# Kernel tuning notes

Hardware: AMD Instinct MI355X
Metric: run time of the kernel (lower is better)

Reference implementation:

```python
import jax, jax.numpy as jnp
import numpy as np

WS = 16          # window_size
SHIFT = 8        # shift_size
HEADS = 6
DIM = 180
CONV_SCALE = 0.01
EPS = 1e-5       # LayerNorm eps (torch default)


def _ln(x, g, b):
    mu = jnp.mean(x, -1, keepdims=True)
    var = jnp.mean((x - mu) ** 2, -1, keepdims=True)
    return (x - mu) / jnp.sqrt(var + EPS) * g + b


def _window_partition(x, ws):
    b, h, w, c = x.shape
    x = x.reshape(b, h // ws, ws, w // ws, ws, c)
    return x.transpose(0, 1, 3, 2, 4, 5).reshape(-1, ws, ws, c)


def _window_reverse(win, ws, h, w):
    b = win.shape[0] // ((h // ws) * (w // ws))
    x = win.reshape(b, h // ws, w // ws, ws, ws, -1)
    return x.transpose(0, 1, 3, 2, 4, 5).reshape(b, h, w, -1)


def _conv2d(x, w, b, pad):
    y = jax.lax.conv_general_dilated(x, w, (1, 1), ((pad, pad), (pad, pad)),
                                     dimension_numbers=('NCHW', 'OIHW', 'NCHW'))
    return y + b[None, :, None, None]


def setup_inputs() -> dict:
    key = jax.random.key(0)
    ks = jax.random.split(key, 12)
    b, h, w = 1, 256, 256
    c = DIM
    hid = int(c * 4.0)
    cr = c // 3     # compress_ratio=3
    sq = c // 30    # squeeze_factor=30
    x = jax.random.normal(ks[0], (b, h * w, c), jnp.float32)

    # relative position index (standard Swin recipe)
    coords = np.stack(np.meshgrid(np.arange(WS), np.arange(WS), indexing='ij')).reshape(2, -1)
    rel = (coords[:, :, None] - coords[:, None, :]).transpose(1, 2, 0)
    rel[:, :, 0] += WS - 1
    rel[:, :, 1] += WS - 1
    rel[:, :, 0] *= 2 * WS - 1
    rpi_sa = jnp.asarray(rel.sum(-1), jnp.int32)  # [ws*ws, ws*ws]

    # shifted-window attention mask
    img = np.zeros((h, w))
    cnt = 0
    for hs in (slice(0, -WS), slice(-WS, -SHIFT), slice(-SHIFT, None)):
        for wsl in (slice(0, -WS), slice(-WS, -SHIFT), slice(-SHIFT, None)):
            img[hs, wsl] = cnt
            cnt += 1
    mw = img.reshape(h // WS, WS, w // WS, WS).transpose(0, 2, 1, 3).reshape(-1, WS * WS)
    am = mw[:, None, :] - mw[:, :, None]
    attn_mask = jnp.asarray(np.where(am != 0, -100.0, 0.0), jnp.float32)  # [nW, n, n]

    def p(k, shape, std=0.02):
        return jax.random.normal(k, shape, jnp.float32) * std

    return dict(
        x=x, h=h, w=w, rpi_sa=rpi_sa, attn_mask=attn_mask,
        norm1_g=jnp.ones((c,), jnp.float32), norm1_b=jnp.zeros((c,), jnp.float32),
        qkv_w=p(ks[1], (c, 3 * c)), qkv_b=jnp.zeros((3 * c,), jnp.float32),
        rpb_table=p(ks[2], ((2 * WS - 1) * (2 * WS - 1), HEADS)),
        proj_w=p(ks[3], (c, c)), proj_b=jnp.zeros((c,), jnp.float32),
        conv1_w=p(ks[4], (cr, c, 3, 3)), conv1_b=jnp.zeros((cr,), jnp.float32),
        conv2_w=p(ks[5], (c, cr, 3, 3)), conv2_b=jnp.zeros((c,), jnp.float32),
        ca1_w=p(ks[6], (sq, c, 1, 1)), ca1_b=jnp.zeros((sq,), jnp.float32),
        ca2_w=p(ks[7], (c, sq, 1, 1)), ca2_b=jnp.zeros((c,), jnp.float32),
        norm2_g=jnp.ones((c,), jnp.float32), norm2_b=jnp.zeros((c,), jnp.float32),
        fc1_w=p(ks[8], (c, hid)), fc1_b=jnp.zeros((hid,), jnp.float32),
        fc2_w=p(ks[9], (hid, c)), fc2_b=jnp.zeros((c,), jnp.float32),
    )


def reference(x, h, w, rpi_sa, attn_mask,
              norm1_g, norm1_b, qkv_w, qkv_b, rpb_table, proj_w, proj_b,
              conv1_w, conv1_b, conv2_w, conv2_b, ca1_w, ca1_b, ca2_w, ca2_b,
              norm2_g, norm2_b, fc1_w, fc1_b, fc2_w, fc2_b):
    b, _, c = x.shape
    shortcut = x
    xn = _ln(x, norm1_g, norm1_b).reshape(b, h, w, c)

    # CAB conv branch (NCHW)
    xi = xn.transpose(0, 3, 1, 2)
    y = _conv2d(xi, conv1_w, conv1_b, 1)
    y = jax.nn.gelu(y, approximate=False)
    y = _conv2d(y, conv2_w, conv2_b, 1)
    ca = jnp.mean(y, axis=(2, 3), keepdims=True)          # AdaptiveAvgPool2d(1)
    ca = jax.nn.relu(_conv2d(ca, ca1_w, ca1_b, 0))
    ca = jax.nn.sigmoid(_conv2d(ca, ca2_w, ca2_b, 0))
    conv_x = (y * ca).transpose(0, 2, 3, 1).reshape(b, h * w, c)

    # shifted window attention
    sx = jnp.roll(xn, (-SHIFT, -SHIFT), (1, 2))
    xw = _window_partition(sx, WS).reshape(-1, WS * WS, c)  # [B_, n, c]
    B_, n, _ = xw.shape
    hd = c // HEADS
    qkv = (xw @ qkv_w + qkv_b).reshape(B_, n, 3, HEADS, hd).transpose(2, 0, 3, 1, 4)
    q, k, v = qkv[0] * hd ** (-0.5), qkv[1], qkv[2]
    attn = jnp.einsum('bhqd,bhkd->bhqk', q, k)
    rpb = rpb_table[rpi_sa.reshape(-1)].reshape(n, n, HEADS).transpose(2, 0, 1)
    attn = attn + rpb[None]
    nw = attn_mask.shape[0]
    attn = attn.reshape(B_ // nw, nw, HEADS, n, n) + attn_mask[None, :, None]
    attn = jax.nn.softmax(attn.reshape(B_, HEADS, n, n), -1)
    out = jnp.einsum('bhqk,bhkd->bhqd', attn, v).transpose(0, 2, 1, 3).reshape(B_, n, c)
    out = out @ proj_w + proj_b
    sx = _window_reverse(out.reshape(-1, WS, WS, c), WS, h, w)
    attn_x = jnp.roll(sx, (SHIFT, SHIFT), (1, 2)).reshape(b, h * w, c)

    x = shortcut + attn_x + conv_x * CONV_SCALE
    xm = _ln(x, norm2_g, norm2_b)
    m = jax.nn.gelu(xm @ fc1_w + fc1_b, approximate=False)
    x = x + (m @ fc2_w + fc2_b)
    return x
```

## Files before the change

### kernel.cpp

```cpp
#include <hip/hip_runtime.h>
#include <hip/hip_bf16.h>
#include <math.h>

#define NTOK 65536
#define C 180
#define KP1 192
#define RCHUNK 32768

typedef __attribute__((ext_vector_type(8))) __bf16 bf16x8;
typedef __attribute__((ext_vector_type(4))) float floatx4;

__device__ __forceinline__ float gelu_f(float v) {
    return 0.5f * v * (1.f + erff(v * 0.7071067811865475f));
}
__device__ __forceinline__ float bflo(unsigned int u) { return __uint_as_float(u << 16); }
__device__ __forceinline__ float bfhi(unsigned int u) { return __uint_as_float(u & 0xffff0000u); }

__device__ __forceinline__ int win2pix(int wrow) {
    int wi = wrow >> 8, ni = wrow & 255;
    int r2 = ((wi >> 4) << 4) | (ni >> 4);
    int c2 = ((wi & 15) << 4) | (ni & 15);
    int r = (r2 + 8) & 255, c = (c2 + 8) & 255;
    return (r << 8) | c;
}

__global__ __launch_bounds__(256) void ln_k(const float* __restrict__ x,
                                            const float* __restrict__ g,
                                            const float* __restrict__ b,
                                            __hip_bfloat16* __restrict__ y) {
    const int wav = threadIdx.x >> 6;
    const int lane = threadIdx.x & 63;
    const int row = blockIdx.x * 4 + wav;
    const float* xr = x + (size_t)row * C;
    float v0 = xr[lane];
    float v1 = xr[lane + 64];
    float v2 = (lane < C - 128) ? xr[lane + 128] : 0.f;
    float sum = v0 + v1 + v2;
    float sq = v0 * v0 + v1 * v1 + v2 * v2;
#pragma unroll
    for (int off = 32; off >= 1; off >>= 1) {
        sum += __shfl_xor(sum, off, 64);
        sq += __shfl_xor(sq, off, 64);
    }
    const float mu = sum * (1.f / C);
    const float var = sq * (1.f / C) - mu * mu;
    const float rstd = rsqrtf(var + 1e-5f);
    __hip_bfloat16* yr = y + (size_t)row * KP1;
#pragma unroll
    for (int e = 0; e < 3; ++e) {
        int col = lane + 64 * e;
        float val = 0.f;
        if (col < C) {
            float vv = (e == 0) ? v0 : (e == 1 ? v1 : v2);
            val = (vv - mu) * rstd * g[col] + b[col];
        }
        yr[col] = __float2bfloat16(val);
    }
}

__device__ __forceinline__ void wconv_item(const float* __restrict__ w,
                                           __hip_bfloat16* __restrict__ wb,
                                           int O, int I, int OCP, int KP, int idx) {
    int tap = idx / (OCP * KP);
    int rem = idx - tap * (OCP * KP);
    int oc = rem / KP, ch = rem - oc * KP;
    float v = (oc < O && ch < I) ? w[((size_t)(oc * I + ch)) * 9 + tap] : 0.f;
    wb[idx] = __float2bfloat16(v);
}
__device__ __forceinline__ void wprep_item(const float* __restrict__ w,
                                           __hip_bfloat16* __restrict__ bt,
                                           int K, int N, int KPd, int idx) {
    int n = idx / KPd, k = idx - n * KPd;
    float v = (n < N && k < K) ? w[(size_t)k * N + n] : 0.f;
    bt[idx] = __float2bfloat16(v);
}
__global__ void prep_all_k(const int* __restrict__ rpi, const float* __restrict__ table,
                           const float* __restrict__ mask,
                           __hip_bfloat16* __restrict__ rpbM,
                           const float* __restrict__ c1w, __hip_bfloat16* __restrict__ wb1,
                           const float* __restrict__ c2w, __hip_bfloat16* __restrict__ wb2,
                           const float* __restrict__ qkvw, __hip_bfloat16* __restrict__ qkvbt,
                           const float* __restrict__ projw, __hip_bfloat16* __restrict__ projbt,
                           const float* __restrict__ f1w, __hip_bfloat16* __restrict__ f1bt,
                           const float* __restrict__ f2w, __hip_bfloat16* __restrict__ f2bt) {
    int idx = blockIdx.x * 256 + threadIdx.x;
    if (idx < 65536) {
        int t = rpi[idx];
        float m1 = mask[(size_t)15 * 65536 + idx];
        float m2 = mask[(size_t)240 * 65536 + idx];
        float m3 = mask[(size_t)255 * 65536 + idx];
#pragma unroll
        for (int h = 0; h < 6; ++h) {
            float base = table[t * 6 + h];
            rpbM[((size_t)(0 * 6 + h)) * 65536 + idx] = __float2bfloat16(base);
            rpbM[((size_t)(1 * 6 + h)) * 65536 + idx] = __float2bfloat16(base + m1);
            rpbM[((size_t)(2 * 6 + h)) * 65536 + idx] = __float2bfloat16(base + m2);
            rpbM[((size_t)(3 * 6 + h)) * 65536 + idx] = __float2bfloat16(base + m3);
        }
        return;
    }
    idx -= 65536;
    if (idx < 110592) { wconv_item(c1w, wb1, 60, 180, 64, 192, idx); return; }
    idx -= 110592;
    if (idx < 110592) { wconv_item(c2w, wb2, 180, 60, 192, 64, idx); return; }
    idx -= 110592;
    if (idx < 122880) { wprep_item(qkvw, qkvbt, 180, 540, 192, idx); return; }
    idx -= 122880;
    if (idx < 36864) { wprep_item(projw, projbt, 180, 180, 192, idx); return; }
    idx -= 36864;
    if (idx < 147456) { wprep_item(f1w, f1bt, 180, 720, 192, idx); return; }
    idx -= 147456;
    if (idx < 147456) { wprep_item(f2w, f2bt, 720, 180, 768, idx); return; }
}

template <int TH, int CINP, int COUT, int OSTR, int ACT, int OUTBF>
__global__ __launch_bounds__(256) void mconv_k(const __hip_bfloat16* __restrict__ in, int istr,
                                               const __hip_bfloat16* __restrict__ wb,
                                               const float* __restrict__ bias,
                                               void* __restrict__ outp) {
    constexpr int MI = TH / 4;
    __shared__ __hip_bfloat16 sP[(TH + 2) * 18 * 40];
    __shared__ __hip_bfloat16 sW[9 * 64 * 40];
    const int tid = threadIdx.x;
    const int tr0 = (blockIdx.x >> 4) * TH, tc0 = (blockIdx.x & 15) * 16;
    const int ocbase = blockIdx.y * 64;
    const int w = tid >> 6, lane = tid & 63, fr = lane & 15, q = lane >> 4;
    constexpr int OCP = ((COUT + 63) / 64) * 64;
    floatx4 acc[MI][4] = {};
    for (int c0 = 0; c0 < CINP; c0 += 32) {
        for (int l = tid; l < (TH + 2) * 18 * 4; l += 256) {
            int pos = l >> 2, part = l & 3;
            int pr = pos / 18, pc = pos - pr * 18;
            int gr = tr0 + pr - 1, gc = tc0 + pc - 1;
            float4 v = make_float4(0.f, 0.f, 0.f, 0.f);
            if (gr >= 0 && gr < 256 && gc >= 0 && gc < 256)
                v = *(const float4*)(in + (size_t)(gr * 256 + gc) * istr + c0 + part * 8);
            *(float4*)(sP + pos * 40 + part * 8) = v;
        }
        for (int l = tid; l < 9 * 64 * 4; l += 256) {
            int part = l & 3, oc = (l >> 2) & 63, tap = l >> 8;
            *(float4*)(sW + tap * 2560 + oc * 40 + part * 8) =
                *(const float4*)(wb + (size_t)(tap * OCP + ocbase + oc) * CINP + c0 + part * 8);
        }
        __syncthreads();
#pragma unroll
        for (int tap = 0; tap < 9; ++tap) {
            const int dy = tap / 3, dx = tap - 3 * (tap / 3);
            bf16x8 af[MI], bw[4];
#pragma unroll
            for (int mi = 0; mi < MI; ++mi) {
                int pr = MI * w + mi + dy, pc = fr + dx;
                af[mi] = *(const bf16x8*)(sP + (pr * 18 + pc) * 40 + q * 8);
            }
#pragma unroll
            for (int nj = 0; nj < 4; ++nj)
                bw[nj] = *(const bf16x8*)(sW + tap * 2560 + (nj * 16 + fr) * 40 + q * 8);
#pragma unroll
            for (int mi = 0; mi < MI; ++mi)
#pragma unroll
                for (int nj = 0; nj < 4; ++nj)
                    acc[mi][nj] =
                        __builtin_amdgcn_mfma_f32_16x16x32_bf16(af[mi], bw[nj], acc[mi][nj], 0, 0, 0);
        }
        __syncthreads();
    }
#pragma unroll
    for (int mi = 0; mi < MI; ++mi) {
#pragma unroll
        for (int r = 0; r < 4; ++r) {
            const int irow = tr0 + MI * w + mi;
            const int icol = tc0 + q * 4 + r;
            const size_t obase = (size_t)(irow * 256 + icol) * OSTR + ocbase;
#pragma unroll
            for (int nj = 0; nj < 4; ++nj) {
                int oc = ocbase + nj * 16 + fr;
                float bv = (oc < COUT) ? bias[oc] : 0.f;
                float v = acc[mi][nj][r] + bv;
                if (ACT) v = gelu_f(v);
                if (OUTBF) {
                    ((__hip_bfloat16*)outp)[obase + nj * 16 + fr] = __float2bfloat16(v);
                } else {
                    if (oc < COUT) ((float*)outp)[obase + nj * 16 + fr] = v;
                }
            }
        }
    }
}

__global__ __launch_bounds__(192) void chansum_k(const float* __restrict__ y2,
                                                 float* __restrict__ partials) {
    const int tid = threadIdx.x;
    if (tid >= C) return;
    const size_t base = (size_t)blockIdx.x * 256 * C;
    float s = 0.f;
    for (int p = 0; p < 256; ++p) s += y2[base + (size_t)p * C + tid];
    partials[blockIdx.x * C + tid] = s;
}

__global__ __launch_bounds__(256) void ca_k(const float* __restrict__ partials,
                                            const float* __restrict__ w1, const float* __restrict__ b1,
                                            const float* __restrict__ w2, const float* __restrict__ b2,
                                            float* __restrict__ scale) {
    __shared__ float mean[C];
    __shared__ float s1[6];
    const int tid = threadIdx.x;
    if (tid < C) {
        float s = 0.f;
        for (int b_ = 0; b_ < 256; ++b_) s += partials[b_ * C + tid];
        mean[tid] = s * (1.f / 65536.f);
    }
    __syncthreads();
    if (tid < 6) {
        float s = b1[tid];
        for (int ch = 0; ch < C; ++ch) s += mean[ch] * w1[tid * C + ch];
        s1[tid] = fmaxf(s, 0.f);
    }
    __syncthreads();
    if (tid < C) {
        float s = b2[tid];
#pragma unroll
        for (int j = 0; j < 6; ++j) s += s1[j] * w2[tid * 6 + j];
        scale[tid] = 1.f / (1.f + __expf(-s));
    }
}

template <int MODE, int BN>
__global__ __launch_bounds__(256) void mgemm_k(const unsigned short* __restrict__ A,
                                               const unsigned short* __restrict__ BT,
                                               const float* __restrict__ bias,
                                               const float* __restrict__ xres,
                                               const float* __restrict__ scale,
                                               void* __restrict__ Cout,
                                               int KPd, int N, int cstride, int rowoff) {
    __shared__ unsigned short As[128 * 40];
    __shared__ unsigned short Bs[BN * 40];
    constexpr int NJ = BN / 32;
    const int tid = threadIdx.x;
    const int m0 = blockIdx.y * 128, n0 = blockIdx.x * BN;
    const int arow_l = tid >> 1;
    const int akofs = (tid & 1) * 16;
    size_t arow;
    if (MODE == 3)
        arow = (size_t)win2pix(rowoff + m0 + arow_l) * KPd;
    else
        arow = (size_t)(m0 + arow_l) * KPd;
    const int brow_l = (BN == 128) ? (tid >> 1) : (tid >> 2);
    const int bkofs = (BN == 128) ? ((tid & 1) * 16) : ((tid & 3) * 8);
    const size_t brow = (size_t)(n0 + brow_l) * KPd;
    const int wave = tid >> 6, lane = tid & 63;
    const int wm = (wave & 1) * 64, wn = (wave >> 1) * (BN / 2);
    const int fr = lane & 15, q = lane >> 4;
    floatx4 acc[4][NJ] = {};
    for (int k0 = 0; k0 < KPd; k0 += 32) {
        if (MODE == 5) {
            const unsigned short* Ap = A + ((size_t)(k0 >> 5) * cstride + (m0 + arow_l)) * 32;
            *(float4*)(&As[arow_l * 40 + akofs]) = *(const float4*)(Ap + akofs);
            *(float4*)(&As[arow_l * 40 + akofs + 8]) = *(const float4*)(Ap + akofs + 8);
        } else {
            *(float4*)(&As[arow_l * 40 + akofs]) = *(const float4*)(A + arow + k0 + akofs);
            *(float4*)(&As[arow_l * 40 + akofs + 8]) = *(const float4*)(A + arow + k0 + akofs + 8);
        }
        if (BN == 128) {
            *(float4*)(&Bs[brow_l * 40 + bkofs]) = *(const float4*)(BT + brow + k0 + bkofs);
            *(float4*)(&Bs[brow_l * 40 + bkofs + 8]) = *(const float4*)(BT + brow + k0 + bkofs + 8);
        } else {
            *(float4*)(&Bs[brow_l * 40 + bkofs]) = *(const float4*)(BT + brow + k0 + bkofs);
        }
        __syncthreads();
        bf16x8 af[4], fB[NJ];
#pragma unroll
        for (int i = 0; i < 4; ++i)
            af[i] = *(const bf16x8*)(&As[(wm + i * 16 + fr) * 40 + q * 8]);
#pragma unroll
        for (int j = 0; j < NJ; ++j)
            fB[j] = *(const bf16x8*)(&Bs[(wn + j * 16 + fr) * 40 + q * 8]);
#pragma unroll
        for (int i = 0; i < 4; ++i)
#pragma unroll
            for (int j = 0; j < NJ; ++j)
                acc[i][j] = __builtin_amdgcn_mfma_f32_16x16x32_bf16(af[i], fB[j], acc[i][j], 0, 0, 0);
        __syncthreads();
    }
#pragma unroll
    for (int i = 0; i < 4; ++i) {
#pragma unroll
        for (int r = 0; r < 4; ++r) {
            const int grow = m0 + wm + i * 16 + q * 4 + r;
            int pix = 0;
            if (MODE == 5) pix = win2pix(rowoff + grow);
#pragma unroll
            for (int j = 0; j < NJ; ++j) {
                const int col = n0 + wn + j * 16 + fr;
                float v = acc[i][j][r];
                if (MODE == 1 || MODE == 3) {
                    if (col < cstride) {
                        float vv = 0.f;
                        if (col < N) {
                            vv = v + bias[col];
                            if (MODE == 1) vv = gelu_f(vv);
                        }
                        ((__hip_bfloat16*)Cout)[(size_t)grow * cstride + col] = __float2bfloat16(vv);
                    }
                } else if (MODE == 2) {
                    if (col < N) {
                        float* o = (float*)Cout;
                        size_t ix = (size_t)grow * 180 + col;
                        o[ix] = v + bias[col] + xres[ix];
                    }
                } else if (MODE == 5) {
                    if (col < N) {
                        float* o = (float*)Cout;
                        size_t ix = (size_t)pix * 180 + col;
                        o[ix] = xres[ix] + v + bias[col] + o[ix] * scale[col] * 0.01f;
                    }
                }
            }
        }
    }
}

__global__ __launch_bounds__(256, 4) void attn7_k(const __hip_bfloat16* __restrict__ qkv,
                                                  const __hip_bfloat16* __restrict__ rpbM,
                                                  __hip_bfloat16* __restrict__ attn_out,
                                                  int wbase, int rows) {
    const int wl = blockIdx.x, h = blockIdx.y;
    const int wig = wbase + wl;
    const int typ = (((wig >> 4) == 15) ? 2 : 0) + (((wig & 15) == 15) ? 1 : 0);
    const int tid = threadIdx.x;
    const int w = tid >> 6, lane = tid & 63;
    const int fr = lane & 15, q = lane >> 4;
    __shared__ __hip_bfloat16 kk[256 * 40];
    __shared__ __hip_bfloat16 vT[32 * 264];

    union UB2 { unsigned int u; __hip_bfloat162 h2; };
    for (int l = tid; l < 256 * 15; l += 256) {
        int key = l / 15, dw_ = l - key * 15;
        const unsigned int* ks =
            (const unsigned int*)(qkv + (size_t)(wl * 256 + key) * 576 + 180 + h * 30);
        *(unsigned int*)(kk + key * 40 + dw_ * 2) = ks[dw_];
        UB2 vv; vv.u = ks[90 + dw_];
        vT[(2 * dw_) * 264 + key] = vv.h2.x;
        vT[(2 * dw_ + 1) * 264 + key] = vv.h2.y;
    }
    *(unsigned int*)(kk + tid * 40 + 30) = 0u;
    for (int l = tid; l < 2 * 264; l += 256) vT[30 * 264 + l] = __float2bfloat16(0.f);
    __syncthreads();

    const int rowbase = wl * 256 + w * 64;
    union U8 { unsigned int u[4]; bf16x8 v; };
    bf16x8 qf[4];
#pragma unroll
    for (int qi = 0; qi < 4; ++qi) {
        const unsigned int* p32 =
            (const unsigned int*)(qkv + (size_t)(rowbase + qi * 16 + fr) * 576 + h * 30);
        U8 t;
#pragma unroll
        for (int jj = 0; jj < 4; ++jj) t.u[jj] = p32[q * 4 + jj];
        qf[qi] = t.v;
    }

    const float SC = 0.18257418583505536f;
    float lsum[4] = {};
    floatx4 o_[4][2] = {};
    const __hip_bfloat16* rpbh = rpbM + ((size_t)(typ * 6 + h)) * 65536;
    const int srcA = fr + ((q & 1) << 5);
    const int srcB = srcA + 16;

    for (int nc = 0; nc < 4; ++nc) {
        bf16x8 kf[4];
#pragma unroll
        for (int ki = 0; ki < 4; ++ki)
            kf[ki] = *(const bf16x8*)(kk + (nc * 64 + ki * 16 + fr) * 40 + q * 8);
        uint2 rb[4][4];
#pragma unroll
        for (int qi = 0; qi < 4; ++qi) {
            const size_t qoff = ((size_t)(w * 64 + qi * 16 + fr)) * 256 + nc * 64 + q * 4;
#pragma unroll
            for (int ki = 0; ki < 4; ++ki)
                rb[qi][ki] = *(const uint2*)(rpbh + qoff + ki * 16);
        }
        unsigned int dw[4][4][2];
#pragma unroll
        for (int qi = 0; qi < 4; ++qi) {
            floatx4 s_[4] = {};
#pragma unroll
            for (int ki = 0; ki < 4; ++ki)
                s_[ki] = __builtin_amdgcn_mfma_f32_16x16x32_bf16(kf[ki], qf[qi], s_[ki], 0, 0, 0);
#pragma unroll
            for (int ki = 0; ki < 4; ++ki) {
                uint2 rbv = rb[qi][ki];
                float b0 = bflo(rbv.x), b1 = bfhi(rbv.x), b2 = bflo(rbv.y), b3 = bfhi(rbv.y);
                float p0 = __expf(fmaf(s_[ki][0], SC, b0));
                float p1 = __expf(fmaf(s_[ki][1], SC, b1));
                float p2 = __expf(fmaf(s_[ki][2], SC, b2));
                float p3 = __expf(fmaf(s_[ki][3], SC, b3));
                lsum[qi] += (p0 + p1) + (p2 + p3);
                __hip_bfloat162 lo = {__float2bfloat16(p0), __float2bfloat16(p1)};
                __hip_bfloat162 hi = {__float2bfloat16(p2), __float2bfloat16(p3)};
                UB2 ul, uh; ul.h2 = lo; uh.h2 = hi;
                dw[ki][qi][0] = ul.u;
                dw[ki][qi][1] = uh.u;
            }
        }
#pragma unroll
        for (int kc = 0; kc < 2; ++kc) {
            bf16x8 pa[4];
#pragma unroll
            for (int mi = 0; mi < 4; ++mi) {
                unsigned g0 = __shfl((int)dw[2 * kc][mi][0], srcA, 64);
                unsigned g1 = __shfl((int)dw[2 * kc][mi][1], srcA, 64);
                unsigned g2 = __shfl((int)dw[2 * kc][mi][0], srcB, 64);
                unsigned g3 = __shfl((int)dw[2 * kc][mi][1], srcB, 64);
                unsigned h0 = __shfl((int)dw[2 * kc + 1][mi][0], srcA, 64);
                unsigned h1 = __shfl((int)dw[2 * kc + 1][mi][1], srcA, 64);
                unsigned h2 = __shfl((int)dw[2 * kc + 1][mi][0], srcB, 64);
                unsigned h3 = __shfl((int)dw[2 * kc + 1][mi][1], srcB, 64);
                U8 t;
                const bool lo = (q < 2);
                t.u[0] = lo ? g0 : h0;
                t.u[1] = lo ? g1 : h1;
                t.u[2] = lo ? g2 : h2;
                t.u[3] = lo ? g3 : h3;
                pa[mi] = t.v;
            }
            bf16x8 vb[2];
#pragma unroll
            for (int dj = 0; dj < 2; ++dj)
                vb[dj] = *(const bf16x8*)(vT + (dj * 16 + fr) * 264 + nc * 64 + kc * 32 + q * 8);
#pragma unroll
            for (int mi = 0; mi < 4; ++mi)
#pragma unroll
                for (int dj = 0; dj < 2; ++dj)
                    o_[mi][dj] =
                        __builtin_amdgcn_mfma_f32_16x16x32_bf16(pa[mi], vb[dj], o_[mi][dj], 0, 0, 0);
        }
    }
#pragma unroll
    for (int qi = 0; qi < 4; ++qi) {
        lsum[qi] += __shfl_xor(lsum[qi], 16, 64);
        lsum[qi] += __shfl_xor(lsum[qi], 32, 64);
    }
    __hip_bfloat16* plane = attn_out + (size_t)h * rows * 32;
#pragma unroll
    for (int mi = 0; mi < 4; ++mi) {
#pragma unroll
        for (int r = 0; r < 4; ++r) {
            float tot = __shfl(lsum[mi], q * 4 + r, 64);
            float inv = 1.f / tot;
            const int row_local = rowbase + mi * 16 + q * 4 + r;
            __hip_bfloat16* orow = plane + (size_t)row_local * 32;
#pragma unroll
            for (int dj = 0; dj < 2; ++dj) {
                int d = dj * 16 + fr;
                float val = (d < 30) ? o_[mi][dj][r] * inv : 0.f;
                orow[d] = __float2bfloat16(val);
            }
        }
    }
}

extern "C" void kernel_launch(void* const* d_in, const int* in_sizes, int n_in, void* d_out,
                              int out_size, void* d_ws, size_t ws_size, hipStream_t stream) {
    (void)in_sizes; (void)n_in; (void)out_size;
    const float* x = (const float*)d_in[0];
    const int* rpi = (const int*)d_in[3];
    const float* mask = (const float*)d_in[4];
    const float* n1g = (const float*)d_in[5];
    const float* n1b = (const float*)d_in[6];
    const float* qkvw = (const float*)d_in[7];
    const float* qkvb = (const float*)d_in[8];
    const float* rpbt = (const float*)d_in[9];
    const float* projw = (const float*)d_in[10];
    const float* projb = (const float*)d_in[11];
    const float* c1w = (const float*)d_in[12];
    const float* c1b = (const float*)d_in[13];
    const float* c2w = (const float*)d_in[14];
    const float* c2b = (const float*)d_in[15];
    const float* ca1w = (const float*)d_in[16];
    const float* ca1b = (const float*)d_in[17];
    const float* ca2w = (const float*)d_in[18];
    const float* ca2b = (const float*)d_in[19];
    const float* n2g = (const float*)d_in[20];
    const float* n2b = (const float*)d_in[21];
    const float* f1w = (const float*)d_in[22];
    const float* f1b = (const float*)d_in[23];
    const float* f2w = (const float*)d_in[24];
    const float* f2b = (const float*)d_in[25];

    float* ws = (float*)d_ws;
    float* out = (float*)d_out;

    const int merged = (ws_size >= 130511616ull) ? 1 : 0;
    const int RATT = merged ? 65536 : 32768;
    const int nck = merged ? 1 : 2;
    const size_t bufCf = merged ? 25165824u : 12582912u;
    const size_t attnCoff = merged ? 18874368u : 9437184u;

    float* xn_f     = ws;
    float* bufC     = xn_f + 6291456;
    float* partials = bufC + bufCf;
    float* scalep   = partials + 46080;
    float* rpbM_f   = scalep + 192;
    float* wb1_f    = rpbM_f + 786432;
    float* wb2_f    = wb1_f + 55296;
    float* qkvbt_f  = wb2_f + 55296;
    float* projbt_f = qkvbt_f + 61440;
    float* f1bt_f   = projbt_f + 18432;
    float* f2bt_f   = f1bt_f + 73728;

    __hip_bfloat16* xn    = (__hip_bfloat16*)xn_f;
    __hip_bfloat16* y1b   = (__hip_bfloat16*)bufC;
    __hip_bfloat16* qkvC  = (__hip_bfloat16*)bufC;
    __hip_bfloat16* attnC = (__hip_bfloat16*)(bufC + attnCoff);
    __hip_bfloat16* h1    = (__hip_bfloat16*)bufC;
    __hip_bfloat16* rpbM   = (__hip_bfloat16*)rpbM_f;
    __hip_bfloat16* wb1    = (__hip_bfloat16*)wb1_f;
    __hip_bfloat16* wb2    = (__hip_bfloat16*)wb2_f;
    __hip_bfloat16* qkvbt  = (__hip_bfloat16*)qkvbt_f;
    __hip_bfloat16* projbt = (__hip_bfloat16*)projbt_f;
    __hip_bfloat16* f1bt   = (__hip_bfloat16*)f1bt_f;
    __hip_bfloat16* f2bt   = (__hip_bfloat16*)f2bt_f;

    prep_all_k<<<(741376 + 255) / 256, 256, 0, stream>>>(rpi, rpbt, mask, rpbM, c1w, wb1, c2w, wb2,
                                                         qkvw, qkvbt, projw, projbt,
                                                         f1w, f1bt, f2w, f2bt);

    ln_k<<<NTOK / 4, 256, 0, stream>>>(x, n1g, n1b, xn);

    mconv_k<8, 192, 60, 64, 1, 1><<<dim3(512, 1), 256, 0, stream>>>(xn, 192, wb1, c1b, y1b);
    mconv_k<16, 64, 180, 180, 0, 0><<<dim3(256, 3), 256, 0, stream>>>(y1b, 64, wb2, c2b, out);
    chansum_k<<<256, 192, 0, stream>>>(out, partials);
    ca_k<<<1, 256, 0, stream>>>(partials, ca1w, ca1b, ca2w, ca2b, scalep);

    for (int ck = 0; ck < nck; ++ck) {
        const int rowoff = ck * RATT;
        mgemm_k<3, 128><<<dim3(5, RATT / 128), 256, 0, stream>>>(
            (const unsigned short*)xn, (const unsigned short*)qkvbt, qkvb, nullptr, nullptr,
            qkvC, 192, 540, 576, rowoff);
        attn7_k<<<dim3(RATT / 256, 6), 256, 0, stream>>>(qkvC, rpbM, attnC, rowoff / 256, RATT);
        mgemm_k<5, 64><<<dim3(3, RATT / 128), 256, 0, stream>>>(
            (const unsigned short*)attnC, (const unsigned short*)projbt, projb, x, scalep,
            out, 192, 180, RATT, rowoff);
    }

    ln_k<<<NTOK / 4, 256, 0, stream>>>(out, n2g, n2b, xn);

    for (int ck = 0; ck < 2; ++ck) {
        const int rowoff = ck * RCHUNK;
        mgemm_k<1, 128><<<dim3(6, RCHUNK / 128), 256, 0, stream>>>(
            (const unsigned short*)(xn + (size_t)rowoff * KP1), (const unsigned short*)f1bt,
            f1b, nullptr, nullptr, h1, 192, 720, 768, 0);
        mgemm_k<2, 64><<<dim3(3, RCHUNK / 128), 256, 0, stream>>>(
            (const unsigned short*)h1, (const unsigned short*)f2bt, f2b,
            out + (size_t)rowoff * 180, nullptr, out + (size_t)rowoff * 180, 768, 180, 180, 0);
    }
}
```

Measured before the change: 716.9 us.

## Swizzle K/V shared layout and double-buffer bias loads in window attention

The attention kernel packs K and transposed V into unpadded shared-memory tiles with an XOR swizzle instead of padded strides. This shrinks LDS use and still avoids bank conflicts. It also prefetches the next key chunk's relative-position bias into a double-buffered register array while the current chunk computes, hoists Q and first-bias loads above the shared-memory fill, and raises the occupancy hint from 4 to 5 blocks. The risk is that the extra registers for double-buffered bias clash with the higher occupancy target and cause spills.

```diff
diff --git a/kernel.cpp b/kernel.cpp
--- a/kernel.cpp
+++ b/kernel.cpp
@@ -319,7 +319,7 @@
     }
 }
 
-__global__ __launch_bounds__(256, 4) void attn7_k(const __hip_bfloat16* __restrict__ qkv,
+__global__ __launch_bounds__(256, 5) void attn8_k(const __hip_bfloat16* __restrict__ qkv,
                                                   const __hip_bfloat16* __restrict__ rpbM,
                                                   __hip_bfloat16* __restrict__ attn_out,
                                                   int wbase, int rows) {
@@ -329,55 +329,77 @@
     const int tid = threadIdx.x;
     const int w = tid >> 6, lane = tid & 63;
     const int fr = lane & 15, q = lane >> 4;
-    __shared__ __hip_bfloat16 kk[256 * 40];
-    __shared__ __hip_bfloat16 vT[32 * 264];
+    __shared__ __hip_bfloat16 kk[256 * 32];
+    __shared__ __hip_bfloat16 vT[32 * 256];
 
     union UB2 { unsigned int u; __hip_bfloat162 h2; };
+    union U8 { unsigned int u[4]; bf16x8 v; };
+
+    const int rowbase = wl * 256 + w * 64;
+    bf16x8 qf[4];
+#pragma unroll
+    for (int qi = 0; qi < 4; ++qi) {
+        const unsigned int* p32 =
+            (const unsigned int*)(qkv + (size_t)(rowbase + qi * 16 + fr) * 576 + h * 30);
+        U8 t;
+#pragma unroll
+        for (int jj = 0; jj < 4; ++jj) t.u[jj] = p32[q * 4 + jj];
+        qf[qi] = t.v;
+    }
+
+    const __hip_bfloat16* rpbh = rpbM + ((size_t)(typ * 6 + h)) * 65536;
+    uint2 rb[2][4][4];
+#pragma unroll
+    for (int qi = 0; qi < 4; ++qi) {
+        const size_t qoff = ((size_t)(w * 64 + qi * 16 + fr)) * 256 + q * 4;
+#pragma unroll
+        for (int ki = 0; ki < 4; ++ki)
+            rb[0][qi][ki] = *(const uint2*)(rpbh + qoff + ki * 16);
+    }
+
     for (int l = tid; l < 256 * 15; l += 256) {
         int key = l / 15, dw_ = l - key * 15;
         const unsigned int* ks =
             (const unsigned int*)(qkv + (size_t)(wl * 256 + key) * 576 + 180 + h * 30);
-        *(unsigned int*)(kk + key * 40 + dw_ * 2) = ks[dw_];
+        unsigned int kv = ks[dw_];
+        *(unsigned int*)((char*)kk + key * 64 + (((dw_ >> 2) ^ (key & 3)) << 4) + ((dw_ & 3) << 2)) = kv;
         UB2 vv; vv.u = ks[90 + dw_];
-        vT[(2 * dw_) * 264 + key] = vv.h2.x;
-        vT[(2 * dw_ + 1) * 264 + key] = vv.h2.y;
-    }
-    *(unsigned int*)(kk + tid * 40 + 30) = 0u;
-    for (int l = tid; l < 2 * 264; l += 256) vT[30 * 264 + l] = __float2bfloat16(0.f);
+        const int d0 = 2 * dw_, d1 = d0 + 1;
+        *(__hip_bfloat16*)((char*)vT + d0 * 512 + (((key >> 3) ^ d0) << 4) + ((key & 7) << 1)) = vv.h2.x;
+        *(__hip_bfloat16*)((char*)vT + d1 * 512 + (((key >> 3) ^ d1) << 4) + ((key & 7) << 1)) = vv.h2.y;
+    }
+    *(unsigned int*)((char*)kk + tid * 64 + ((3 ^ (tid & 3)) << 4) + 12) = 0u;
+    for (int l = tid; l < 2 * 256; l += 256) {
+        int d = 30 + (l >> 8), key = l & 255;
+        *(__hip_bfloat16*)((char*)vT + d * 512 + (((key >> 3) ^ d) << 4) + ((key & 7) << 1)) =
+            __float2bfloat16(0.f);
+    }
     __syncthreads();
-
-    const int rowbase = wl * 256 + w * 64;
-    union U8 { unsigned int u[4]; bf16x8 v; };
-    bf16x8 qf[4];
-#pragma unroll
-    for (int qi = 0; qi < 4; ++qi) {
-        const unsigned int* p32 =
-            (const unsigned int*)(qkv + (size_t)(rowbase + qi * 16 + fr) * 576 + h * 30);
-        U8 t;
-#pragma unroll
-        for (int jj = 0; jj < 4; ++jj) t.u[jj] = p32[q * 4 + jj];
-        qf[qi] = t.v;
-    }
 
     const float SC = 0.18257418583505536f;
     float lsum[4] = {};
     floatx4 o_[4][2] = {};
-    const __hip_bfloat16* rpbh = rpbM + ((size_t)(typ * 6 + h)) * 65536;
     const int srcA = fr + ((q & 1) << 5);
     const int srcB = srcA + 16;
 
+#pragma unroll
     for (int nc = 0; nc < 4; ++nc) {
+        const int cur = nc & 1;
+        if (nc < 3) {
+#pragma unroll
+            for (int qi = 0; qi < 4; ++qi) {
+                const size_t qoff =
+                    ((size_t)(w * 64 + qi * 16 + fr)) * 256 + (nc + 1) * 64 + q * 4;
+#pragma unroll
+                for (int ki = 0; ki < 4; ++ki)
+                    rb[cur ^ 1][qi][ki] = *(const uint2*)(rpbh + qoff + ki * 16);
+            }
+        }
         bf16x8 kf[4];
 #pragma unroll
-        for (int ki = 0; ki < 4; ++ki)
-            kf[ki] = *(const bf16x8*)(kk + (nc * 64 + ki * 16 + fr) * 40 + q * 8);
-        uint2 rb[4][4];
-#pragma unroll
-        for (int qi = 0; qi < 4; ++qi) {
-            const size_t qoff = ((size_t)(w * 64 + qi * 16 + fr)) * 256 + nc * 64 + q * 4;
-#pragma unroll
-            for (int ki = 0; ki < 4; ++ki)
-                rb[qi][ki] = *(const uint2*)(rpbh + qoff + ki * 16);
+        for (int ki = 0; ki < 4; ++ki) {
+            const int key = nc * 64 + ki * 16 + fr;
+            kf[ki] = *(const bf16x8*)((const char*)kk + key * 64 + ((q ^ (fr & 3)) << 4));
         }
         unsigned int dw[4][4][2];
 #pragma unroll
@@ -388,7 +410,7 @@
                 s_[ki] = __builtin_amdgcn_mfma_f32_16x16x32_bf16(kf[ki], qf[qi], s_[ki], 0, 0, 0);
 #pragma unroll
             for (int ki = 0; ki < 4; ++ki) {
-                uint2 rbv = rb[qi][ki];
+                uint2 rbv = rb[cur][qi][ki];
                 float b0 = bflo(rbv.x), b1 = bfhi(rbv.x), b2 = bflo(rbv.y), b3 = bfhi(rbv.y);
                 float p0 = __expf(fmaf(s_[ki][0], SC, b0));
                 float p1 = __expf(fmaf(s_[ki][1], SC, b1));
@@ -425,8 +447,11 @@
             }
             bf16x8 vb[2];
 #pragma unroll
-            for (int dj = 0; dj < 2; ++dj)
-                vb[dj] = *(const bf16x8*)(vT + (dj * 16 + fr) * 264 + nc * 64 + kc * 32 + q * 8);
+            for (int dj = 0; dj < 2; ++dj) {
+                const int d = dj * 16 + fr;
+                vb[dj] = *(const bf16x8*)((const char*)vT + d * 512 +
+                                          (((nc * 8 + kc * 4 + q) ^ d) << 4));
+            }
 #pragma unroll
             for (int mi = 0; mi < 4; ++mi)
 #pragma unroll
@@ -537,7 +562,7 @@
         mgemm_k<3, 128><<<dim3(5, RATT / 128), 256, 0, stream>>>(
             (const unsigned short*)xn, (const unsigned short*)qkvbt, qkvb, nullptr, nullptr,
             qkvC, 192, 540, 576, rowoff);
-        attn7_k<<<dim3(RATT / 256, 6), 256, 0, stream>>>(qkvC, rpbM, attnC, rowoff / 256, RATT);
+        attn8_k<<<dim3(RATT / 256, 6), 256, 0, stream>>>(qkvC, rpbM, attnC, rowoff / 256, RATT);
         mgemm_k<5, 64><<<dim3(3, RATT / 128), 256, 0, stream>>>(
             (const unsigned short*)attnC, (const unsigned short*)projbt, projb, x, scalep,
             out, 192, 180, RATT, rowoff);
```

Result: slower. 804.1 us (+12.2%).
